# Kernel tuning notes

Measured on AMD Instinct MI355X. Metric: run time of the kernel, lower is better.

## Reference

```python
import jax, jax.numpy as jnp
import numpy as np

VOCAB = 32000
HID = 1024
HEADS = 16
HEAD_DIM = HID // HEADS
LAYERS = 8
INTER = 4 * HID
ROPE_BASE = 100000.0
EPS = 1e-5


def setup_inputs() -> dict:
    key = jax.random.key(0)
    ks = jax.random.split(key, 12)
    s = 0.02
    inp = {
        'input_ids': jax.random.randint(ks[0], (2, 2048), 0, VOCAB),
        'embed_W': jax.random.normal(ks[1], (VOCAB, HID), jnp.float32) * s,
        'Wq': jax.random.normal(ks[2], (LAYERS, HID, HID), jnp.float32) * s,
        'Wk': jax.random.normal(ks[3], (LAYERS, HID, HID), jnp.float32) * s,
        'Wv': jax.random.normal(ks[4], (LAYERS, HID, HID), jnp.float32) * s,
        'Wo': jax.random.normal(ks[5], (LAYERS, HID, HID), jnp.float32) * s,
        'Wg': jax.random.normal(ks[6], (LAYERS, HID, INTER), jnp.float32) * s,
        'Wu': jax.random.normal(ks[7], (LAYERS, HID, INTER), jnp.float32) * s,
        'Wd': jax.random.normal(ks[8], (LAYERS, INTER, HID), jnp.float32) * s,
        'norm1_w': jnp.ones((LAYERS, HID), jnp.float32),
        'norm2_w': jnp.ones((LAYERS, HID), jnp.float32),
        'final_norm_w': jnp.ones((HID,), jnp.float32),
        'head_W': jax.random.normal(ks[9], (HID, VOCAB), jnp.float32) * s,
    }
    return inp


def rms_norm(x, w):
    return x * jax.lax.rsqrt(jnp.mean(x * x, axis=-1, keepdims=True) + EPS) * w


def rope_tables(seq_len):
    freq = 1.0 / (ROPE_BASE ** (jnp.arange(0, HEAD_DIM, 2, dtype=jnp.float32) / HEAD_DIM))
    ang = jnp.arange(seq_len, dtype=jnp.float32)[:, None] * freq  # [S, d/2]
    cos = jnp.concatenate([jnp.cos(ang), jnp.cos(ang)], axis=-1)  # [S, d]
    sin = jnp.concatenate([jnp.sin(ang), jnp.sin(ang)], axis=-1)
    return cos, sin


def rotate_half(x):
    h = x.shape[-1] // 2
    return jnp.concatenate([-x[..., h:], x[..., :h]], axis=-1)


def apply_rope(q, k, cos, sin):
    # q,k: [B,S,H,D]; cos,sin: [S,D] -> broadcast over heads via [:,None,:]
    c = cos[:, None, :]
    s = sin[:, None, :]
    return q * c + rotate_half(q) * s, k * c + rotate_half(k) * s


def attention(x, wq, wk, wv, wo, cos, sin, causal_mask):
    B, S, _ = x.shape
    q = (x @ wq).reshape(B, S, HEADS, HEAD_DIM)
    k = (x @ wk).reshape(B, S, HEADS, HEAD_DIM)
    v = (x @ wv).reshape(B, S, HEADS, HEAD_DIM)
    q, k = apply_rope(q, k, cos, sin)
    scores = jnp.einsum('bqhd,bkhd->bhqk', q, k) / np.sqrt(HEAD_DIM)
    scores = jnp.clip(scores, -1000.0, 1000.0)
    scores = jnp.where(causal_mask, jnp.finfo(scores.dtype).min, scores)
    w = jax.nn.softmax(scores.astype(jnp.float32), axis=-1).astype(q.dtype)
    w = jnp.clip(w, 0.0, 1.0)
    ctx = jnp.einsum('bhqk,bkhd->bqhd', w, v).reshape(B, S, HID)
    return ctx @ wo


def reference(input_ids, embed_W, Wq, Wk, Wv, Wo, Wg, Wu, Wd, norm1_w, norm2_w, final_norm_w, head_W):
    B, S = input_ids.shape
    h = embed_W[input_ids]  # [B,S,HID]
    cos, sin = rope_tables(S)
    causal_mask = jnp.triu(jnp.ones((S, S), bool), k=1)[None, None]
    for l in range(LAYERS):
        h = h + attention(rms_norm(h, norm1_w[l]), Wq[l], Wk[l], Wv[l], Wo[l], cos, sin, causal_mask)
        hn = rms_norm(h, norm2_w[l])
        h = h + (jax.nn.silu(hn @ Wg[l]) * (hn @ Wu[l])) @ Wd[l]
    h = rms_norm(h, final_norm_w)
    logits = h @ head_W
    return logits, h
```

## Files before the change

kernel.cpp:

```cpp
#include <hip/hip_runtime.h>

#define T_TOK 4096
#define SEQ   2048
#define HID   1024
#define NH    16
#define HD    64
#define INTER 4096
#define NLAYER 8
#define VOCAB 32000

typedef short short8 __attribute__((ext_vector_type(8)));
typedef float f32x4  __attribute__((ext_vector_type(4)));

__device__ __forceinline__ unsigned short f2bf(float f){
  unsigned int u = __builtin_bit_cast(unsigned int, f);
  u += 0x7fffu + ((u >> 16) & 1u);
  return (unsigned short)(u >> 16);
}
__device__ __forceinline__ float bf2f(unsigned short b){
  unsigned int u = ((unsigned int)b) << 16;
  return __builtin_bit_cast(float, u);
}

#define GLOAD_LDS16(gsrc, ldst) \
  __builtin_amdgcn_global_load_lds((const __attribute__((address_space(1))) void*)(gsrc), \
                                   (__attribute__((address_space(3))) void*)(ldst), 16, 0, 0)

__global__ __launch_bounds__(256) void embed_kernel(const int* __restrict__ ids,
                                                    const float* __restrict__ W,
                                                    float* __restrict__ h){
  int i = blockIdx.x * 256 + threadIdx.x;
  int t = i >> 8, c = i & 255;
  ((float4*)h)[i] = ((const float4*)(W + (size_t)ids[t] * HID))[c];
}

__global__ __launch_bounds__(256) void rope_tab_kernel(float* __restrict__ cosT,
                                                       float* __restrict__ sinT){
  int i = blockIdx.x * 256 + threadIdx.x;
  int s = i >> 5, f = i & 31;
  float inv = expf(-((2.0f * (float)f) / 64.0f) * logf(100000.0f));
  float ang = (float)s * inv;
  cosT[i] = cosf(ang);
  sinT[i] = sinf(ang);
}

__global__ __launch_bounds__(256) void rmsnorm_kernel(const float* __restrict__ h,
                                                      const float* __restrict__ w,
                                                      unsigned short* __restrict__ out,
                                                      float* hcopy){
  int t = blockIdx.x, tid = threadIdx.x;
  float4 v = ((const float4*)(h + (size_t)t * HID))[tid];
  float ss = v.x*v.x + v.y*v.y + v.z*v.z + v.w*v.w;
  #pragma unroll
  for (int m = 1; m < 64; m <<= 1) ss += __shfl_xor(ss, m);
  __shared__ float red[4];
  if ((tid & 63) == 0) red[tid >> 6] = ss;
  __syncthreads();
  float r = rsqrtf((red[0] + red[1] + red[2] + red[3]) * (1.0f / HID) + 1e-5f);
  float4 wv = ((const float4*)w)[tid];
  float nx = v.x * r * wv.x;
  float ny = v.y * r * wv.y;
  float nz = v.z * r * wv.z;
  float nw = v.w * r * wv.w;
  ushort4 o;
  o.x = f2bf(nx); o.y = f2bf(ny); o.z = f2bf(nz); o.w = f2bf(nw);
  ((ushort4*)(out + (size_t)t * HID))[tid] = o;
  if (hcopy){
    float4 hv; hv.x = nx; hv.y = ny; hv.z = nz; hv.w = nw;
    ((float4*)(hcopy + (size_t)t * HID))[tid] = hv;
  }
}

__global__ __launch_bounds__(256) void rope_kernel(unsigned short* __restrict__ q,
                                                   unsigned short* __restrict__ k,
                                                   const float* __restrict__ cosT,
                                                   const float* __restrict__ sinT){
  int i = blockIdx.x * 256 + threadIdx.x;
  int t = i >> 9, rem = i & 511;
  int hh = rem >> 5, f = rem & 31;
  int s = t & (SEQ - 1);
  float c = cosT[s * 32 + f], sn = sinT[s * 32 + f];
  size_t base = (size_t)t * HID + hh * HD + f;
  float q0 = bf2f(q[base]), q1 = bf2f(q[base + 32]);
  q[base]      = f2bf(q0 * c - q1 * sn);
  q[base + 32] = f2bf(q1 * c + q0 * sn);
  float k0 = bf2f(k[base]), k1 = bf2f(k[base + 32]);
  k[base]      = f2bf(k0 * c - k1 * sn);
  k[base + 32] = f2bf(k1 * c + k0 * sn);
}

__global__ __launch_bounds__(256) void convert_w_kernel(const float* __restrict__ W,
                                                        unsigned short* __restrict__ Wt,
                                                        int K, int N){
  __shared__ unsigned short t_lds[64][72];
  W  += (size_t)blockIdx.z * K * N;
  Wt += (size_t)blockIdx.z * K * N;
  const int n0 = blockIdx.x * 64, k0 = blockIdx.y * 64;
  const int tid = threadIdx.x;
  const int tr = tid >> 4, tc = tid & 15;
  #pragma unroll
  for (int i = 0; i < 4; ++i){
    int kk = tr + i * 16;
    float4 v = *(const float4*)(W + (size_t)(k0 + kk) * N + n0 + tc * 4);
    t_lds[tc*4+0][kk] = f2bf(v.x);
    t_lds[tc*4+1][kk] = f2bf(v.y);
    t_lds[tc*4+2][kk] = f2bf(v.z);
    t_lds[tc*4+3][kk] = f2bf(v.w);
  }
  __syncthreads();
  const int n = tid >> 2, cp = tid & 3;
  #pragma unroll
  for (int j = 0; j < 2; ++j){
    int c = cp * 2 + j;
    uint4 d = *(const uint4*)(&t_lds[n][c * 8]);
    *(uint4*)(Wt + (size_t)(n0 + n) * K + k0 + c * 8) = d;
  }
}

__device__ __forceinline__ void gemm_core(const unsigned short* __restrict__ A,
                                          const unsigned short* __restrict__ Bt,
                                          int K, int m0, int n0,
                                          unsigned short* As, unsigned short* Bs,
                                          f32x4 (&acc)[4][4]){
  const int tid = threadIdx.x;
  const int lane = tid & 63, w = tid >> 6;
  const int l15 = lane & 15, g = lane >> 4;
  const int wr = w >> 1, wc = w & 1;
  const int srow = lane >> 2;
  const int soff = (lane & 3) << 3;

  #pragma unroll
  for (int m = 0; m < 4; ++m)
    #pragma unroll
    for (int n = 0; n < 4; ++n)
      #pragma unroll
      for (int i = 0; i < 4; ++i) acc[m][n][i] = 0.0f;

  for (int kk = 0; kk < K; kk += 32){
    __syncthreads();
    GLOAD_LDS16(A  + (size_t)(m0 +      w*16 + srow) * K + kk + soff, As + (w*16) * 32);
    GLOAD_LDS16(A  + (size_t)(m0 + 64 + w*16 + srow) * K + kk + soff, As + (64 + w*16) * 32);
    GLOAD_LDS16(Bt + (size_t)(n0 +      w*16 + srow) * K + kk + soff, Bs + (w*16) * 32);
    GLOAD_LDS16(Bt + (size_t)(n0 + 64 + w*16 + srow) * K + kk + soff, Bs + (64 + w*16) * 32);
    __syncthreads();
    short8 a[4], b[4];
    #pragma unroll
    for (int m = 0; m < 4; ++m)
      a[m] = *(const short8*)(As + (wr*64 + m*16 + l15) * 32 + g*8);
    #pragma unroll
    for (int n = 0; n < 4; ++n)
      b[n] = *(const short8*)(Bs + (wc*64 + n*16 + l15) * 32 + g*8);
    #pragma unroll
    for (int m = 0; m < 4; ++m)
      #pragma unroll
      for (int n = 0; n < 4; ++n)
        acc[m][n] = __builtin_amdgcn_mfma_f32_16x16x32_bf16(a[m], b[n], acc[m][n], 0, 0, 0);
  }
}

template<int MODE>
__device__ __forceinline__ void gemm_epi(const f32x4 (&acc)[4][4], void* Cout,
                                         const float* __restrict__ resid,
                                         int N, int m0, int n0, int ldt){
  const int tid = threadIdx.x;
  const int lane = tid & 63, w = tid >> 6;
  const int l15 = lane & 15, g = lane >> 4;
  const int wr = w >> 1, wc = w & 1;
  #pragma unroll
  for (int m = 0; m < 4; ++m){
    #pragma unroll
    for (int n = 0; n < 4; ++n){
      int row0 = m0 + wr * 64 + m * 16 + g * 4;
      int col  = n0 + wc * 64 + n * 16 + l15;
      #pragma unroll
      for (int i = 0; i < 4; ++i){
        float v = acc[m][n][i];
        if (MODE == 0){
          ((unsigned short*)Cout)[(size_t)(row0 + i) * N + col] = f2bf(v);
        } else if (MODE == 1){
          size_t idx = (size_t)(row0 + i) * N + col;
          ((float*)Cout)[idx] = resid[idx] + v;
        } else if (MODE == 2){
          ((unsigned short*)Cout)[(size_t)col * ldt + (row0 + i)] = f2bf(v);
        } else {
          __builtin_nontemporal_store(v, &((float*)Cout)[(size_t)(row0 + i) * N + col]);
        }
      }
    }
  }
}

template<int MODE>
__global__ __launch_bounds__(256) void gemm_bf16(const unsigned short* __restrict__ A,
                                                 const unsigned short* __restrict__ Bt,
                                                 void* Cout, const float* resid,
                                                 int K, int N, int ldt){
  __shared__ unsigned short As[128 * 32];
  __shared__ unsigned short Bs[128 * 32];
  f32x4 acc[4][4];
  gemm_core(A, Bt, K, blockIdx.x * 128, blockIdx.y * 128, As, Bs, acc);
  gemm_epi<MODE>(acc, Cout, resid, N, blockIdx.x * 128, blockIdx.y * 128, ldt);
}

__global__ __launch_bounds__(256) void gemm_qkv(const unsigned short* __restrict__ A,
                                                const unsigned short* __restrict__ BtQ,
                                                const unsigned short* __restrict__ BtK,
                                                const unsigned short* __restrict__ BtV,
                                                unsigned short* qb, unsigned short* kb,
                                                unsigned short* vt){
  __shared__ unsigned short As[128 * 32];
  __shared__ unsigned short Bs[128 * 32];
  const int nb = blockIdx.y, sel = nb >> 3, n0 = (nb & 7) * 128;
  const unsigned short* Bt = (sel == 0) ? BtQ : (sel == 1) ? BtK : BtV;
  f32x4 acc[4][4];
  gemm_core(A, Bt, HID, blockIdx.x * 128, n0, As, Bs, acc);
  if (sel == 0)      gemm_epi<0>(acc, qb, nullptr, HID, blockIdx.x * 128, n0, 0);
  else if (sel == 1) gemm_epi<0>(acc, kb, nullptr, HID, blockIdx.x * 128, n0, 0);
  else               gemm_epi<2>(acc, vt, nullptr, HID, blockIdx.x * 128, n0, T_TOK);
}

__global__ __launch_bounds__(256) void gemm_gu(const unsigned short* __restrict__ A,
                                               const unsigned short* __restrict__ BtG,
                                               const unsigned short* __restrict__ BtU,
                                               unsigned short* gb, unsigned short* ub){
  __shared__ unsigned short As[128 * 32];
  __shared__ unsigned short Bs[128 * 32];
  const int nb = blockIdx.y, sel = nb >> 5, n0 = (nb & 31) * 128;
  f32x4 acc[4][4];
  gemm_core(A, sel ? BtU : BtG, HID, blockIdx.x * 128, n0, As, Bs, acc);
  gemm_epi<0>(acc, sel ? ub : gb, nullptr, INTER, blockIdx.x * 128, n0, 0);
}

__global__ __launch_bounds__(256, 2) void gemm_f32b(const unsigned short* __restrict__ A,
                                                    const float* __restrict__ Bw,
                                                    float* __restrict__ Cout,
                                                    int M, int N, int K){
  __shared__ unsigned short As[128 * 32];
  __shared__ unsigned short Bs[128 * 32];
  const int tid = threadIdx.x;
  const int lane = tid & 63, wid = tid >> 6;
  const int l15 = lane & 15, g = lane >> 4;
  const int wr = wid >> 1, wc = wid & 1;
  const int m0 = blockIdx.x * 128, n0 = blockIdx.y * 128;
  const int bcol = tid & 127, bhalf = tid >> 7;
  f32x4 acc[4][4];
  #pragma unroll
  for (int m = 0; m < 4; ++m)
    #pragma unroll
    for (int n = 0; n < 4; ++n)
      #pragma unroll
      for (int i = 0; i < 4; ++i) acc[m][n][i] = 0.0f;
  for (int kk = 0; kk < K; kk += 32){
    __syncthreads();
    #pragma unroll
    for (int cc = 0; cc < 2; ++cc){
      int c = tid + cc * 256;
      int row = c >> 2, kc = (c & 3) << 3;
      uint4 d = *(const uint4*)(A + (size_t)(m0 + row) * K + kk + kc);
      *(uint4*)(&As[row * 32 + kc]) = d;
    }
    {
      const float* bp = Bw + (size_t)(kk + bhalf * 16) * N + n0 + bcol;
      float f[16];
      #pragma unroll
      for (int j = 0; j < 16; ++j) f[j] = bp[(size_t)j * N];
      unsigned int pk[8];
      #pragma unroll
      for (int j = 0; j < 8; ++j)
        pk[j] = (unsigned int)f2bf(f[2*j]) | ((unsigned int)f2bf(f[2*j+1]) << 16);
      int sw = (bcol >> 1) & 3;
      int c0 = ((bhalf << 1)     ) ^ sw;
      int c1 = ((bhalf << 1) | 1 ) ^ sw;
      uint4 w0; w0.x = pk[0]; w0.y = pk[1]; w0.z = pk[2]; w0.w = pk[3];
      uint4 w1; w1.x = pk[4]; w1.y = pk[5]; w1.z = pk[6]; w1.w = pk[7];
      *(uint4*)(&Bs[bcol * 32 + c0 * 8]) = w0;
      *(uint4*)(&Bs[bcol * 32 + c1 * 8]) = w1;
    }
    __syncthreads();
    short8 a[4], b[4];
    #pragma unroll
    for (int m = 0; m < 4; ++m)
      a[m] = *(const short8*)(&As[(wr*64 + m*16 + l15) * 32 + g*8]);
    #pragma unroll
    for (int n = 0; n < 4; ++n){
      int col = wc*64 + n*16 + l15;
      b[n] = *(const short8*)(&Bs[col * 32 + (g ^ ((col >> 1) & 3)) * 8]);
    }
    #pragma unroll
    for (int m = 0; m < 4; ++m)
      #pragma unroll
      for (int n = 0; n < 4; ++n)
        acc[m][n] = __builtin_amdgcn_mfma_f32_16x16x32_bf16(a[m], b[n], acc[m][n], 0, 0, 0);
  }
  #pragma unroll
  for (int m = 0; m < 4; ++m)
    #pragma unroll
    for (int n = 0; n < 4; ++n){
      int row0 = m0 + wr*64 + m*16 + g*4;
      int col  = n0 + wc*64 + n*16 + l15;
      #pragma unroll
      for (int i = 0; i < 4; ++i)
        Cout[(size_t)(row0 + i) * N + col] = acc[m][n][i];
    }
}

__global__ __launch_bounds__(256) void attn_kernel(const unsigned short* __restrict__ q,
                                                   const unsigned short* __restrict__ k,
                                                   const unsigned short* __restrict__ vt,
                                                   unsigned short* __restrict__ ctx){
  const int tid = threadIdx.x;
  const int lane = tid & 63, w = tid >> 6;
  const int l15 = lane & 15, g = lane >> 4;
  const int bx = (int)gridDim.x - 1 - (int)blockIdx.x;
  const int q0 = bx * 128 + w * 32;
  const int hh = blockIdx.y;
  const int tb = blockIdx.z * SEQ;

  __shared__ unsigned short Ks[128][72];
  __shared__ unsigned short Vs[64][136];
  __shared__ unsigned short Ps[4][16][136];

  short8 qa[2][2];
  #pragma unroll
  for (int qs = 0; qs < 2; ++qs)
    #pragma unroll
    for (int kd = 0; kd < 2; ++kd)
      qa[qs][kd] = *(const short8*)(q + (size_t)(tb + q0 + qs*16 + l15) * HID + hh*HD + kd*32 + g*8);

  float m_run[2][4], l_run[2][4];
  f32x4 o_acc[2][4];
  #pragma unroll
  for (int qs = 0; qs < 2; ++qs)
    #pragma unroll
    for (int i = 0; i < 4; ++i){ m_run[qs][i] = -1e30f; l_run[qs][i] = 0.0f; }
  #pragma unroll
  for (int qs = 0; qs < 2; ++qs)
    #pragma unroll
    for (int dt = 0; dt < 4; ++dt)
      #pragma unroll
      for (int i = 0; i < 4; ++i) o_acc[qs][dt][i] = 0.0f;

  const int krow = tid >> 1, khf = (tid & 1) * 32;
  const int vrow = tid >> 2, vq  = (tid & 3) * 32;

  for (int kt = 0; kt <= bx; ++kt){
    const int kv0 = kt * 128;
    __syncthreads();
    {
      const unsigned short* kp = k + (size_t)(tb + kv0 + krow) * HID + hh*HD + khf;
      #pragma unroll
      for (int j = 0; j < 4; ++j)
        *(uint4*)(&Ks[krow][khf + j*8]) = *(const uint4*)(kp + j*8);
      const unsigned short* vp = vt + (size_t)(hh*HD + vrow) * T_TOK + tb + kv0 + vq;
      #pragma unroll
      for (int j = 0; j < 4; ++j)
        *(uint4*)(&Vs[vrow][vq + j*8]) = *(const uint4*)(vp + j*8);
    }
    __syncthreads();
    const int nct = (kt < bx) ? 8 : (2 * w + 2);
    const int nks = nct >> 1;

    #pragma unroll
    for (int qs = 0; qs < 2; ++qs){
      float pv[8][4];
      #pragma unroll
      for (int ct = 0; ct < 8; ++ct){
        if (ct < nct){
          f32x4 scv;
          #pragma unroll
          for (int i = 0; i < 4; ++i) scv[i] = 0.0f;
          scv = __builtin_amdgcn_mfma_f32_16x16x32_bf16(qa[qs][0],
                  *(const short8*)(&Ks[ct*16 + l15][g*8]), scv, 0, 0, 0);
          scv = __builtin_amdgcn_mfma_f32_16x16x32_bf16(qa[qs][1],
                  *(const short8*)(&Ks[ct*16 + l15][32 + g*8]), scv, 0, 0, 0);
          #pragma unroll
          for (int i = 0; i < 4; ++i){
            float s = scv[i] * 0.125f;
            s = fminf(fmaxf(s, -1000.0f), 1000.0f);
            int row = q0 + qs*16 + g*4 + i;
            int col = kv0 + ct*16 + l15;
            pv[ct][i] = (col > row) ? -1e30f : s;
          }
        } else {
          #pragma unroll
          for (int i = 0; i < 4; ++i) pv[ct][i] = -1e30f;
        }
      }
      #pragma unroll
      for (int i = 0; i < 4; ++i){
        float mx = pv[0][i];
        #pragma unroll
        for (int ct = 1; ct < 8; ++ct) mx = fmaxf(mx, pv[ct][i]);
        #pragma unroll
        for (int msk = 1; msk < 16; msk <<= 1) mx = fmaxf(mx, __shfl_xor(mx, msk));
        if (!__all(mx <= m_run[qs][i] + 8.0f)){
          float mnew = fmaxf(m_run[qs][i], mx);
          float scale = __expf(m_run[qs][i] - mnew);
          m_run[qs][i] = mnew;
          l_run[qs][i] *= scale;
          #pragma unroll
          for (int dt = 0; dt < 4; ++dt) o_acc[qs][dt][i] *= scale;
        }
        float psum = 0.0f;
        #pragma unroll
        for (int ct = 0; ct < 8; ++ct){
          if (ct < nct){
            float p = __expf(pv[ct][i] - m_run[qs][i]);
            pv[ct][i] = p; psum += p;
          } else pv[ct][i] = 0.0f;
        }
        #pragma unroll
        for (int msk = 1; msk < 16; msk <<= 1) psum += __shfl_xor(psum, msk);
        l_run[qs][i] += psum;
      }
      #pragma unroll
      for (int ct = 0; ct < 8; ++ct)
        if (ct < nct)
          #pragma unroll
          for (int i = 0; i < 4; ++i)
            Ps[w][g*4 + i][ct*16 + l15] = f2bf(pv[ct][i]);
      #pragma unroll
      for (int ks = 0; ks < 4; ++ks){
        if (ks < nks){
          short8 vb[4];
          #pragma unroll
          for (int dt = 0; dt < 4; ++dt)
            vb[dt] = *(const short8*)(&Vs[dt*16 + l15][ks*32 + g*8]);
          short8 ap = *(const short8*)(&Ps[w][l15][ks*32 + g*8]);
          #pragma unroll
          for (int dt = 0; dt < 4; ++dt)
            o_acc[qs][dt] = __builtin_amdgcn_mfma_f32_16x16x32_bf16(ap, vb[dt], o_acc[qs][dt], 0, 0, 0);
        }
      }
    }
  }
  #pragma unroll
  for (int qs = 0; qs < 2; ++qs)
    #pragma unroll
    for (int dt = 0; dt < 4; ++dt)
      #pragma unroll
      for (int i = 0; i < 4; ++i){
        float o = o_acc[qs][dt][i] / l_run[qs][i];
        ctx[(size_t)(tb + q0 + qs*16 + g*4 + i) * HID + hh*HD + dt*16 + l15] = f2bf(o);
      }
}

__global__ __launch_bounds__(256) void silu_mul_kernel(unsigned short* __restrict__ gbuf,
                                                       const unsigned short* __restrict__ ubuf){
  int i = blockIdx.x * 256 + threadIdx.x;
  ushort4 gv = ((const ushort4*)gbuf)[i];
  ushort4 uv = ((const ushort4*)ubuf)[i];
  ushort4 o;
  float x;
  x = bf2f(gv.x); o.x = f2bf((x / (1.0f + __expf(-x))) * bf2f(uv.x));
  x = bf2f(gv.y); o.y = f2bf((x / (1.0f + __expf(-x))) * bf2f(uv.y));
  x = bf2f(gv.z); o.z = f2bf((x / (1.0f + __expf(-x))) * bf2f(uv.z));
  x = bf2f(gv.w); o.w = f2bf((x / (1.0f + __expf(-x))) * bf2f(uv.w));
  ((ushort4*)gbuf)[i] = o;
}

extern "C" void kernel_launch(void* const* d_in, const int* in_sizes, int n_in,
                              void* d_out, int out_size, void* d_ws, size_t ws_size,
                              hipStream_t stream){
  const int*   ids    = (const int*)d_in[0];
  const float* embedW = (const float*)d_in[1];
  const float* Wq = (const float*)d_in[2];
  const float* Wk = (const float*)d_in[3];
  const float* Wv = (const float*)d_in[4];
  const float* Wo = (const float*)d_in[5];
  const float* Wg = (const float*)d_in[6];
  const float* Wu = (const float*)d_in[7];
  const float* Wd = (const float*)d_in[8];
  const float* n1 = (const float*)d_in[9];
  const float* n2 = (const float*)d_in[10];
  const float* nf = (const float*)d_in[11];
  const float* Wh = (const float*)d_in[12];
  float* out = (float*)d_out;

  char* scb = (char*)d_out;
  unsigned short* qb  = (unsigned short*)(scb + 0);
  unsigned short* kb  = (unsigned short*)(scb + 8388608);
  unsigned short* vtb = (unsigned short*)(scb + 16777216);
  unsigned short* ctx = (unsigned short*)(scb + 25165824);
  unsigned short* gb  = (unsigned short*)(scb + 33554432);
  unsigned short* ub  = (unsigned short*)(scb + 67108864);
  float* cosT = (float*)(scb + 100663296);
  float* sinT = (float*)(scb + 100925440);
  float* h_fallback   = (float*)(scb + 104857600);
  unsigned short* WtQ = (unsigned short*)(scb + 134217728);
  unsigned short* WtK = (unsigned short*)(scb + 150994944);
  unsigned short* WtV = (unsigned short*)(scb + 167772160);
  unsigned short* WtO = (unsigned short*)(scb + 184549376);
  unsigned short* WtG = (unsigned short*)(scb + 201326592);
  unsigned short* WtU = (unsigned short*)(scb + 268435456);
  unsigned short* WtD = (unsigned short*)(scb + 335544320);

  unsigned short* xn = (unsigned short*)d_ws;
  float* h = (ws_size >= 25165824u) ? (float*)((char*)d_ws + 8388608) : h_fallback;
  unsigned short* WhT = (ws_size >= 90701824u)
                      ? (unsigned short*)((char*)d_ws + 25165824) : nullptr;

  convert_w_kernel<<<dim3(16, 16, 8), 256, 0, stream>>>(Wq, WtQ, HID, HID);
  convert_w_kernel<<<dim3(16, 16, 8), 256, 0, stream>>>(Wk, WtK, HID, HID);
  convert_w_kernel<<<dim3(16, 16, 8), 256, 0, stream>>>(Wv, WtV, HID, HID);
  convert_w_kernel<<<dim3(16, 16, 8), 256, 0, stream>>>(Wo, WtO, HID, HID);
  convert_w_kernel<<<dim3(64, 16, 8), 256, 0, stream>>>(Wg, WtG, HID, INTER);
  convert_w_kernel<<<dim3(64, 16, 8), 256, 0, stream>>>(Wu, WtU, HID, INTER);
  convert_w_kernel<<<dim3(16, 64, 8), 256, 0, stream>>>(Wd, WtD, INTER, HID);
  if (WhT)
    convert_w_kernel<<<dim3(500, 16, 1), 256, 0, stream>>>(Wh, WhT, HID, VOCAB);

  embed_kernel<<<4096, 256, 0, stream>>>(ids, embedW, h);
  rope_tab_kernel<<<256, 256, 0, stream>>>(cosT, sinT);

  for (int l = 0; l < NLAYER; ++l){
    rmsnorm_kernel<<<4096, 256, 0, stream>>>(h, n1 + l*HID, xn, nullptr);
    gemm_qkv<<<dim3(32, 24), 256, 0, stream>>>(xn, WtQ + (size_t)l*HID*HID,
                                               WtK + (size_t)l*HID*HID,
                                               WtV + (size_t)l*HID*HID, qb, kb, vtb);
    rope_kernel<<<8192, 256, 0, stream>>>(qb, kb, cosT, sinT);
    attn_kernel<<<dim3(16, 16, 2), 256, 0, stream>>>(qb, kb, vtb, ctx);
    gemm_bf16<1><<<dim3(32, 8), 256, 0, stream>>>(ctx, WtO + (size_t)l*HID*HID,
                                                  h, h, HID, HID, 0);
    rmsnorm_kernel<<<4096, 256, 0, stream>>>(h, n2 + l*HID, xn, nullptr);
    gemm_gu<<<dim3(32, 64), 256, 0, stream>>>(xn, WtG + (size_t)l*HID*INTER,
                                              WtU + (size_t)l*HID*INTER, gb, ub);
    silu_mul_kernel<<<16384, 256, 0, stream>>>(gb, ub);
    gemm_bf16<1><<<dim3(32, 8), 256, 0, stream>>>(gb, WtD + (size_t)l*HID*INTER,
                                                  h, h, INTER, HID, 0);
  }

  rmsnorm_kernel<<<4096, 256, 0, stream>>>(h, nf, xn, out + 131072000);
  if (WhT)
    gemm_bf16<3><<<dim3(32, 250), 256, 0, stream>>>(xn, WhT, out, nullptr, HID, VOCAB, 0);
  else
    gemm_f32b<<<dim3(32, 250), 256, 0, stream>>>(xn, Wh, out, T_TOK, VOCAB, HID);
}
```

Before: 3.984 ms.

## Swizzle GEMM LDS, remap blocks across XCDs, retile and prefetch attention

The GEMM core XOR-swizzles the 16-byte chunks it stores into LDS and reads back, to cut LDS bank conflicts on the MFMA operand loads. All GEMM kernels remap block indices so consecutive tiles land on the same XCD, for better L2 reuse. The softmax scale of 1/8 moves from the attention kernel into the RoPE kernel. Attention switches from 128-wide to 64-wide KV tiles, prefetching the next tile into registers while computing the current one, and skips tiles that are fully masked. The XCD remap assumes the grid size is a multiple of 8, and smaller KV tiles mean more barriers per query block.

```diff
diff --git a/kernel.cpp b/kernel.cpp
--- a/kernel.cpp
+++ b/kernel.cpp
@@ -25,6 +25,14 @@
 #define GLOAD_LDS16(gsrc, ldst) \
   __builtin_amdgcn_global_load_lds((const __attribute__((address_space(1))) void*)(gsrc), \
                                    (__attribute__((address_space(3))) void*)(ldst), 16, 0, 0)
+
+__device__ __forceinline__ void xcd_remap(int& bx, int& by){
+  int nx = gridDim.x, n = nx * gridDim.y;
+  int f = by * nx + bx;
+  int cpx = n >> 3;
+  f = (f & 7) * cpx + (f >> 3);
+  bx = f % nx; by = f / nx;
+}
 
 __global__ __launch_bounds__(256) void embed_kernel(const int* __restrict__ ids,
                                                     const float* __restrict__ W,
@@ -82,8 +90,8 @@
   float c = cosT[s * 32 + f], sn = sinT[s * 32 + f];
   size_t base = (size_t)t * HID + hh * HD + f;
   float q0 = bf2f(q[base]), q1 = bf2f(q[base + 32]);
-  q[base]      = f2bf(q0 * c - q1 * sn);
-  q[base + 32] = f2bf(q1 * c + q0 * sn);
+  q[base]      = f2bf((q0 * c - q1 * sn) * 0.125f);
+  q[base + 32] = f2bf((q1 * c + q0 * sn) * 0.125f);
   float k0 = bf2f(k[base]), k1 = bf2f(k[base + 32]);
   k[base]      = f2bf(k0 * c - k1 * sn);
   k[base + 32] = f2bf(k1 * c + k0 * sn);
@@ -127,7 +135,8 @@
   const int l15 = lane & 15, g = lane >> 4;
   const int wr = w >> 1, wc = w & 1;
   const int srow = lane >> 2;
-  const int soff = (lane & 3) << 3;
+  const int schunk = (((lane & 3) ^ ((srow >> 1) & 3)) << 3);
+  const int sx = (l15 >> 1) & 3;
 
   #pragma unroll
   for (int m = 0; m < 4; ++m)
@@ -138,18 +147,18 @@
 
   for (int kk = 0; kk < K; kk += 32){
     __syncthreads();
-    GLOAD_LDS16(A  + (size_t)(m0 +      w*16 + srow) * K + kk + soff, As + (w*16) * 32);
-    GLOAD_LDS16(A  + (size_t)(m0 + 64 + w*16 + srow) * K + kk + soff, As + (64 + w*16) * 32);
-    GLOAD_LDS16(Bt + (size_t)(n0 +      w*16 + srow) * K + kk + soff, Bs + (w*16) * 32);
-    GLOAD_LDS16(Bt + (size_t)(n0 + 64 + w*16 + srow) * K + kk + soff, Bs + (64 + w*16) * 32);
+    GLOAD_LDS16(A  + (size_t)(m0 +      w*16 + srow) * K + kk + schunk, As + (w*16) * 32);
+    GLOAD_LDS16(A  + (size_t)(m0 + 64 + w*16 + srow) * K + kk + schunk, As + (64 + w*16) * 32);
+    GLOAD_LDS16(Bt + (size_t)(n0 +      w*16 + srow) * K + kk + schunk, Bs + (w*16) * 32);
+    GLOAD_LDS16(Bt + (size_t)(n0 + 64 + w*16 + srow) * K + kk + schunk, Bs + (64 + w*16) * 32);
     __syncthreads();
     short8 a[4], b[4];
     #pragma unroll
     for (int m = 0; m < 4; ++m)
-      a[m] = *(const short8*)(As + (wr*64 + m*16 + l15) * 32 + g*8);
+      a[m] = *(const short8*)(As + (wr*64 + m*16 + l15) * 32 + ((g ^ sx) << 3));
     #pragma unroll
     for (int n = 0; n < 4; ++n)
-      b[n] = *(const short8*)(Bs + (wc*64 + n*16 + l15) * 32 + g*8);
+      b[n] = *(const short8*)(Bs + (wc*64 + n*16 + l15) * 32 + ((g ^ sx) << 3));
     #pragma unroll
     for (int m = 0; m < 4; ++m)
       #pragma unroll
@@ -197,9 +206,11 @@
                                                  int K, int N, int ldt){
   __shared__ unsigned short As[128 * 32];
   __shared__ unsigned short Bs[128 * 32];
+  int bx = blockIdx.x, by = blockIdx.y;
+  xcd_remap(bx, by);
   f32x4 acc[4][4];
-  gemm_core(A, Bt, K, blockIdx.x * 128, blockIdx.y * 128, As, Bs, acc);
-  gemm_epi<MODE>(acc, Cout, resid, N, blockIdx.x * 128, blockIdx.y * 128, ldt);
+  gemm_core(A, Bt, K, bx * 128, by * 128, As, Bs, acc);
+  gemm_epi<MODE>(acc, Cout, resid, N, bx * 128, by * 128, ldt);
 }
 
 __global__ __launch_bounds__(256) void gemm_qkv(const unsigned short* __restrict__ A,
@@ -210,13 +221,15 @@
                                                 unsigned short* vt){
   __shared__ unsigned short As[128 * 32];
   __shared__ unsigned short Bs[128 * 32];
-  const int nb = blockIdx.y, sel = nb >> 3, n0 = (nb & 7) * 128;
+  int bx = blockIdx.x, by = blockIdx.y;
+  xcd_remap(bx, by);
+  const int sel = by >> 3, n0 = (by & 7) * 128;
   const unsigned short* Bt = (sel == 0) ? BtQ : (sel == 1) ? BtK : BtV;
   f32x4 acc[4][4];
-  gemm_core(A, Bt, HID, blockIdx.x * 128, n0, As, Bs, acc);
-  if (sel == 0)      gemm_epi<0>(acc, qb, nullptr, HID, blockIdx.x * 128, n0, 0);
-  else if (sel == 1) gemm_epi<0>(acc, kb, nullptr, HID, blockIdx.x * 128, n0, 0);
-  else               gemm_epi<2>(acc, vt, nullptr, HID, blockIdx.x * 128, n0, T_TOK);
+  gemm_core(A, Bt, HID, bx * 128, n0, As, Bs, acc);
+  if (sel == 0)      gemm_epi<0>(acc, qb, nullptr, HID, bx * 128, n0, 0);
+  else if (sel == 1) gemm_epi<0>(acc, kb, nullptr, HID, bx * 128, n0, 0);
+  else               gemm_epi<2>(acc, vt, nullptr, HID, bx * 128, n0, T_TOK);
 }
 
 __global__ __launch_bounds__(256) void gemm_gu(const unsigned short* __restrict__ A,
@@ -225,10 +238,12 @@
                                                unsigned short* gb, unsigned short* ub){
   __shared__ unsigned short As[128 * 32];
   __shared__ unsigned short Bs[128 * 32];
-  const int nb = blockIdx.y, sel = nb >> 5, n0 = (nb & 31) * 128;
+  int bx = blockIdx.x, by = blockIdx.y;
+  xcd_remap(bx, by);
+  const int sel = by >> 5, n0 = (by & 31) * 128;
   f32x4 acc[4][4];
-  gemm_core(A, sel ? BtU : BtG, HID, blockIdx.x * 128, n0, As, Bs, acc);
-  gemm_epi<0>(acc, sel ? ub : gb, nullptr, INTER, blockIdx.x * 128, n0, 0);
+  gemm_core(A, sel ? BtU : BtG, HID, bx * 128, n0, As, Bs, acc);
+  gemm_epi<0>(acc, sel ? ub : gb, nullptr, INTER, bx * 128, n0, 0);
 }
 
 __global__ __launch_bounds__(256, 2) void gemm_f32b(const unsigned short* __restrict__ A,
@@ -316,9 +331,9 @@
   const int hh = blockIdx.y;
   const int tb = blockIdx.z * SEQ;
 
-  __shared__ unsigned short Ks[128][72];
-  __shared__ unsigned short Vs[64][136];
-  __shared__ unsigned short Ps[4][16][136];
+  __shared__ unsigned short Ks[64][72];
+  __shared__ unsigned short Vs[64][72];
+  __shared__ unsigned short Ps[4][16][72];
 
   short8 qa[2][2];
   #pragma unroll
@@ -340,31 +355,38 @@
       #pragma unroll
       for (int i = 0; i < 4; ++i) o_acc[qs][dt][i] = 0.0f;
 
-  const int krow = tid >> 1, khf = (tid & 1) * 32;
-  const int vrow = tid >> 2, vq  = (tid & 3) * 32;
-
-  for (int kt = 0; kt <= bx; ++kt){
-    const int kv0 = kt * 128;
+  const int ntile = 2 * bx + 2;
+  const int srow = tid >> 2, sc = (tid & 3) * 16;
+  const unsigned short* kbase = k  + (size_t)(tb + srow) * HID + hh*HD + sc;
+  const unsigned short* vbase = vt + (size_t)(hh*HD + srow) * T_TOK + tb + sc;
+
+  uint4 kreg[2], vreg[2];
+  kreg[0] = *(const uint4*)(kbase);     kreg[1] = *(const uint4*)(kbase + 8);
+  vreg[0] = *(const uint4*)(vbase);     vreg[1] = *(const uint4*)(vbase + 8);
+
+  for (int kt = 0; kt < ntile; ++kt){
+    const int kv0 = kt * 64;
     __syncthreads();
-    {
-      const unsigned short* kp = k + (size_t)(tb + kv0 + krow) * HID + hh*HD + khf;
-      #pragma unroll
-      for (int j = 0; j < 4; ++j)
-        *(uint4*)(&Ks[krow][khf + j*8]) = *(const uint4*)(kp + j*8);
-      const unsigned short* vp = vt + (size_t)(hh*HD + vrow) * T_TOK + tb + kv0 + vq;
-      #pragma unroll
-      for (int j = 0; j < 4; ++j)
-        *(uint4*)(&Vs[vrow][vq + j*8]) = *(const uint4*)(vp + j*8);
-    }
+    *(uint4*)(&Ks[srow][sc])     = kreg[0];
+    *(uint4*)(&Ks[srow][sc + 8]) = kreg[1];
+    *(uint4*)(&Vs[srow][sc])     = vreg[0];
+    *(uint4*)(&Vs[srow][sc + 8]) = vreg[1];
     __syncthreads();
-    const int nct = (kt < bx) ? 8 : (2 * w + 2);
+    if (kt + 1 < ntile){
+      const unsigned short* kp = kbase + (size_t)(kv0 + 64) * HID;
+      const unsigned short* vp = vbase + (kv0 + 64);
+      kreg[0] = *(const uint4*)(kp);     kreg[1] = *(const uint4*)(kp + 8);
+      vreg[0] = *(const uint4*)(vp);     vreg[1] = *(const uint4*)(vp + 8);
+    }
+    const int nct = min(4, ((q0 + 31 - kv0) >> 4) + 1);
+    if (nct <= 0) continue;
     const int nks = nct >> 1;
 
     #pragma unroll
     for (int qs = 0; qs < 2; ++qs){
-      float pv[8][4];
-      #pragma unroll
-      for (int ct = 0; ct < 8; ++ct){
+      float pv[4][4];
+      #pragma unroll
+      for (int ct = 0; ct < 4; ++ct){
         if (ct < nct){
           f32x4 scv;
           #pragma unroll
@@ -375,8 +397,7 @@
                   *(const short8*)(&Ks[ct*16 + l15][32 + g*8]), scv, 0, 0, 0);
           #pragma unroll
           for (int i = 0; i < 4; ++i){
-            float s = scv[i] * 0.125f;
-            s = fminf(fmaxf(s, -1000.0f), 1000.0f);
+            float s = fminf(fmaxf(scv[i], -1000.0f), 1000.0f);
             int row = q0 + qs*16 + g*4 + i;
             int col = kv0 + ct*16 + l15;
             pv[ct][i] = (col > row) ? -1e30f : s;
@@ -388,9 +409,7 @@
       }
       #pragma unroll
       for (int i = 0; i < 4; ++i){
-        float mx = pv[0][i];
-        #pragma unroll
-        for (int ct = 1; ct < 8; ++ct) mx = fmaxf(mx, pv[ct][i]);
+        float mx = fmaxf(fmaxf(pv[0][i], pv[1][i]), fmaxf(pv[2][i], pv[3][i]));
         #pragma unroll
         for (int msk = 1; msk < 16; msk <<= 1) mx = fmaxf(mx, __shfl_xor(mx, msk));
         if (!__all(mx <= m_run[qs][i] + 8.0f)){
@@ -403,7 +422,7 @@
         }
         float psum = 0.0f;
         #pragma unroll
-        for (int ct = 0; ct < 8; ++ct){
+        for (int ct = 0; ct < 4; ++ct){
           if (ct < nct){
             float p = __expf(pv[ct][i] - m_run[qs][i]);
             pv[ct][i] = p; psum += p;
@@ -414,22 +433,20 @@
         l_run[qs][i] += psum;
       }
       #pragma unroll
-      for (int ct = 0; ct < 8; ++ct)
+      for (int ct = 0; ct < 4; ++ct)
         if (ct < nct)
           #pragma unroll
           for (int i = 0; i < 4; ++i)
             Ps[w][g*4 + i][ct*16 + l15] = f2bf(pv[ct][i]);
       #pragma unroll
-      for (int ks = 0; ks < 4; ++ks){
+      for (int ks = 0; ks < 2; ++ks){
         if (ks < nks){
-          short8 vb[4];
-          #pragma unroll
-          for (int dt = 0; dt < 4; ++dt)
-            vb[dt] = *(const short8*)(&Vs[dt*16 + l15][ks*32 + g*8]);
           short8 ap = *(const short8*)(&Ps[w][l15][ks*32 + g*8]);
           #pragma unroll
-          for (int dt = 0; dt < 4; ++dt)
-            o_acc[qs][dt] = __builtin_amdgcn_mfma_f32_16x16x32_bf16(ap, vb[dt], o_acc[qs][dt], 0, 0, 0);
+          for (int dt = 0; dt < 4; ++dt){
+            short8 vb = *(const short8*)(&Vs[dt*16 + l15][ks*32 + g*8]);
+            o_acc[qs][dt] = __builtin_amdgcn_mfma_f32_16x16x32_bf16(ap, vb, o_acc[qs][dt], 0, 0, 0);
+          }
         }
       }
     }
```

Result: slower. 4.728 ms (+18.7%).
